# Performance work log

Measured on AMD Instinct MI355X. Metric: run time of the kernel, lower is better.

Reference implementation:

```python
import jax, jax.numpy as jnp
import numpy as np

B, T, D, H = 32, 2048, 1024, 128


def setup_inputs() -> dict:
    key = jax.random.key(0)
    ks = jax.random.split(key, 7)
    s = 1.0 / np.sqrt(D)
    return {
        "x": jax.random.normal(ks[0], (B, T, D), dtype=jnp.float32),
        "Wk": jax.random.normal(ks[1], (D, H), dtype=jnp.float32) * s,
        "bk": jax.random.normal(ks[2], (H,), dtype=jnp.float32) * 0.01,
        "Wq": jax.random.normal(ks[3], (D, H), dtype=jnp.float32) * s,
        "bq": jax.random.normal(ks[4], (H,), dtype=jnp.float32) * 0.01,
        "Wv": jax.random.normal(ks[5], (D, H), dtype=jnp.float32) * s,
        "bv": jax.random.normal(ks[6], (H,), dtype=jnp.float32) * 0.01,
    }


def reference(x, Wk, bk, Wq, bq, Wv, bv):
    # Single causal attention head. NOTE faithful quirk: scores = K @ Q^T.
    k = x @ Wk + bk  # [B,T,H]
    q = x @ Wq + bq  # [B,T,H]
    v = x @ Wv + bv  # [B,T,H]
    scale = k.shape[-1] ** -0.5
    wei = jnp.einsum("bth,bsh->bts", k, q) * scale  # [B,T,T], K on the left
    t = x.shape[1]
    causal = jnp.tril(jnp.ones((t, t), dtype=bool))
    wei = jnp.where(causal, wei, -jnp.inf)
    wei = jax.nn.softmax(wei, axis=-1)
    # dropout is eval-mode identity (deterministic reference)
    out = jnp.einsum("bts,bsh->bth", wei, v)  # [B,T,H]
    return out
```

## Files before the change

kernel.cpp:

```cpp
#include <hip/hip_runtime.h>
#include <hip/hip_bf16.h>
#include <stdint.h>

typedef __bf16 bf16;
typedef __bf16 bf16x8 __attribute__((ext_vector_type(8)));
typedef __bf16 bf16x4 __attribute__((ext_vector_type(4)));
typedef float f32x4 __attribute__((ext_vector_type(4)));
typedef float f32x8 __attribute__((ext_vector_type(8)));

#define BB 32
#define TT 2048
#define DD 1024
#define HH 128
#define SCALE 0.08838834764831845f
#define LOG2E 1.4426950408889634f
#define KS (SCALE * LOG2E)

__device__ __forceinline__ void gl_lds16(const bf16* g, bf16* l) {
  __builtin_amdgcn_global_load_lds((__attribute__((address_space(1))) const void*)g,
                                   (__attribute__((address_space(3))) void*)l,
                                   16, 0, 0);
}

__global__ __launch_bounds__(256) void prep_w(const float* __restrict__ Wk,
                                              const float* __restrict__ Wq,
                                              const float* __restrict__ Wv,
                                              const float* __restrict__ bk,
                                              const float* __restrict__ bq,
                                              const float* __restrict__ bv,
                                              bf16* __restrict__ Wt,
                                              float* __restrict__ bcat) {
  int tid = blockIdx.x * 256 + threadIdx.x;
  if (tid < 384) {
    int mat = tid >> 7, h = tid & 127;
    float bb = (mat == 0) ? bk[h] : (mat == 1) ? bq[h] : bv[h];
    bcat[tid] = (mat == 0) ? bb * KS : bb;
  }
  int mat = tid >> 14;
  int r = tid & 16383;
  int h = r & 127;
  int d0 = (r >> 7) << 3;
  const float* W = (mat == 0) ? Wk : (mat == 1) ? Wq : Wv;
  const float ks = (mat == 0) ? KS : 1.0f;
  bf16x8 v;
#pragma unroll
  for (int i = 0; i < 8; ++i) v[i] = (bf16)(W[(size_t)(d0 + i) * HH + h] * ks);
  *(bf16x8*)(Wt + ((size_t)mat * HH + h) * DD + d0) = v;
}

__global__ __launch_bounds__(512, 2) void qkv_proj(
    const float* __restrict__ x, const bf16* __restrict__ Wt,
    const float* __restrict__ bcat,
    bf16* __restrict__ kb, bf16* __restrict__ qb, bf16* __restrict__ Vt) {
  const int bid = blockIdx.x;
  const int tid = threadIdx.x;
  const int lane = tid & 63;
  const int w = tid >> 6;
  const int wr = w >> 2, wc = w & 3;
  const int l15 = lane & 15, l4 = lane >> 4;
  const size_t row0 = (size_t)bid * 256;
  const int colbase = wc * 96;
  const int rowbase = wr * 128;

  __shared__ __attribute__((aligned(16))) bf16 As[2][256][40];
  __shared__ __attribute__((aligned(16))) bf16 Ws[2][384 * 32];

  const int sxr = tid >> 1, sxh = (tid & 1) * 16;

  f32x4 acc[8][6];
#pragma unroll
  for (int m = 0; m < 8; ++m)
#pragma unroll
    for (int n = 0; n < 6; ++n) acc[m][n] = f32x4{0.f, 0.f, 0.f, 0.f};

  auto stage_w = [&](int buf, int k0) {
#pragma unroll
    for (int i = 0; i < 3; ++i) {
      int base = i * 512 + (w << 6);
      int L = base + lane;
      int col = L >> 2, j = L & 3;
      const bf16* src = Wt + (size_t)col * DD + k0 + ((j ^ ((col >> 1) & 3)) << 3);
      gl_lds16(src, &Ws[buf][0] + (size_t)base * 8);
    }
  };
  auto write_x = [&](int buf, f32x8 a0, f32x8 a1) {
    bf16x8 t0, t1;
#pragma unroll
    for (int i = 0; i < 8; ++i) { t0[i] = (bf16)a0[i]; t1[i] = (bf16)a1[i]; }
    *(bf16x8*)&As[buf][sxr][sxh] = t0;
    *(bf16x8*)&As[buf][sxr][sxh + 8] = t1;
  };

  {
    const float* src = x + (row0 + sxr) * DD + sxh;
    f32x8 a0 = *(const f32x8*)src;
    f32x8 a1 = *(const f32x8*)(src + 8);
    stage_w(0, 0);
    write_x(0, a0, a1);
  }
  __syncthreads();

  for (int step = 0; step < 32; ++step) {
    const int cur = step & 1;
    const int k0 = step * 32;

    f32x8 a0, a1;
    if (step < 31) {
      const float* src = x + (row0 + sxr) * DD + k0 + 32 + sxh;
      a0 = *(const f32x8*)src;
      a1 = *(const f32x8*)(src + 8);
      stage_w(cur ^ 1, k0 + 32);
    }

    bf16x8 bfr[6];
#pragma unroll
    for (int n = 0; n < 6; ++n) {
      int col = colbase + n * 16 + l15;
      bfr[n] = *(const bf16x8*)&Ws[cur][col * 32 + ((l4 ^ ((col >> 1) & 3)) << 3)];
    }
#pragma unroll
    for (int m = 0; m < 8; ++m) {
      int r = rowbase + m * 16 + l15;
      bf16x8 afm = *(const bf16x8*)&As[cur][r][l4 * 8];
#pragma unroll
      for (int n = 0; n < 6; ++n)
        acc[m][n] = __builtin_amdgcn_mfma_f32_16x16x32_bf16(afm, bfr[n],
                                                            acc[m][n], 0, 0, 0);
    }

    if (step < 31) write_x(cur ^ 1, a0, a1);
    __syncthreads();
  }

  float bvv[6];
#pragma unroll
  for (int n = 0; n < 6; ++n) bvv[n] = bcat[colbase + n * 16 + l15];

  const int bidx = bid >> 3;
  const int tloc0 = (bid & 7) * 256;
#pragma unroll
  for (int m = 0; m < 8; ++m)
#pragma unroll
    for (int n = 0; n < 6; ++n) {
      int col = colbase + n * 16 + l15;
      int mat = col >> 7;
      int hcol = col & 127;
      int rloc = rowbase + m * 16 + l4 * 4;
      if (mat == 2) {
        bf16x4 v4;
#pragma unroll
        for (int e = 0; e < 4; ++e) v4[e] = (bf16)(acc[m][n][e] + bvv[n]);
        *(bf16x4*)(Vt + ((size_t)bidx * HH + hcol) * TT + tloc0 + rloc) = v4;
      } else {
        bf16* dst = (mat == 0) ? kb : qb;
#pragma unroll
        for (int e = 0; e < 4; ++e)
          dst[(row0 + rloc + e) * HH + hcol] = (bf16)(acc[m][n][e] + bvv[n]);
      }
    }
}

__global__ __launch_bounds__(256, 3) void attn(const bf16* __restrict__ kb,
                                               const bf16* __restrict__ qb,
                                               const bf16* __restrict__ Vt,
                                               float* __restrict__ out) {
  const int bid = blockIdx.x;
  const int b = bid & 31;
  const int p = bid >> 5;
  const int tid = threadIdx.x;
  const int lane = tid & 63;
  const int w = tid >> 6;
  const int l15 = lane & 15, l4 = lane >> 4;

  __shared__ __attribute__((aligned(16))) bf16 Es[64 * 128];
  __shared__ __attribute__((aligned(16))) bf16 Vs[128 * 64];
  __shared__ __attribute__((aligned(16))) bf16 Ps[4][16 * 72];

  for (int job = 0; job < 2; ++job) {
    const int tile = job ? p : (31 - p);
    const int t0 = tile * 64;

    bf16x8 af[4];
    {
      const bf16* kp = kb + ((size_t)b * TT + t0 + w * 16 + l15) * HH + l4 * 8;
#pragma unroll
      for (int kc = 0; kc < 4; ++kc) af[kc] = *(const bf16x8*)(kp + kc * 32);
    }

    f32x4 o[8];
#pragma unroll
    for (int j = 0; j < 8; ++j) o[j] = f32x4{0.f, 0.f, 0.f, 0.f};
    float mrow[4], lrow[4];
#pragma unroll
    for (int e = 0; e < 4; ++e) { mrow[e] = -1e30f; lrow[e] = 0.f; }

    const int nst = tile + 1;
    for (int jt = 0; jt < nst; ++jt) {
      const int s0 = jt * 64;
      {
        const bf16* Eg = qb + ((size_t)b * TT + s0) * HH;
#pragma unroll
        for (int it = 0; it < 4; ++it) {
          int L = w * 256 + it * 64 + lane;
          int er = L >> 4, ec = L & 15;
          int ecs = ec ^ (er & 7);
          gl_lds16(Eg + er * HH + ecs * 8, Es + (size_t)(w * 256 + it * 64) * 8);
        }
        const bf16* Vg = Vt + (size_t)b * HH * TT + s0;
#pragma unroll
        for (int it = 0; it < 4; ++it) {
          int L = w * 256 + it * 64 + lane;
          int vr = L >> 3, vc = L & 7;
          int vcs = vc ^ (vr & 7);
          gl_lds16(Vg + (size_t)vr * TT + vcs * 8, Vs + (size_t)(w * 256 + it * 64) * 8);
        }
      }
      __syncthreads();

      f32x4 s[4];
#pragma unroll
      for (int j = 0; j < 4; ++j) s[j] = f32x4{0.f, 0.f, 0.f, 0.f};
#pragma unroll
      for (int kc = 0; kc < 4; ++kc) {
        bf16x8 ef[4];
#pragma unroll
        for (int fn = 0; fn < 4; ++fn) {
          int er = fn * 16 + l15;
          int c = kc * 4 + l4;
          int cs = c ^ (er & 7);
          ef[fn] = *(const bf16x8*)&Es[er * 128 + cs * 8];
        }
#pragma unroll
        for (int fn = 0; fn < 4; ++fn)
          s[fn] = __builtin_amdgcn_mfma_f32_16x16x32_bf16(af[kc], ef[fn],
                                                          s[fn], 0, 0, 0);
      }

      if (s0 + 63 > t0 + w * 16) {
#pragma unroll
        for (int fn = 0; fn < 4; ++fn)
#pragma unroll
          for (int e = 0; e < 4; ++e) {
            int tg = t0 + w * 16 + l4 * 4 + e;
            int sg = s0 + fn * 16 + l15;
            if (sg > tg) s[fn][e] = -1e30f;
          }
      }

      float mx[4];
#pragma unroll
      for (int e = 0; e < 4; ++e) {
        float m = fmaxf(fmaxf(s[0][e], s[1][e]), fmaxf(s[2][e], s[3][e]));
#pragma unroll
        for (int d = 1; d < 16; d <<= 1) m = fmaxf(m, __shfl_xor(m, d));
        mx[e] = m;
      }
      float g = fmaxf(fmaxf(mx[0] - mrow[0], mx[1] - mrow[1]),
                      fmaxf(mx[2] - mrow[2], mx[3] - mrow[3]));
      if (!__all(g <= 8.0f)) {
#pragma unroll
        for (int e = 0; e < 4; ++e) {
          float mn = fmaxf(mrow[e], mx[e]);
          float rsc = exp2f(mrow[e] - mn);
          lrow[e] *= rsc;
#pragma unroll
          for (int fh = 0; fh < 8; ++fh) o[fh][e] *= rsc;
          mrow[e] = mn;
        }
      }
#pragma unroll
      for (int e = 0; e < 4; ++e) {
        float ps = 0.f;
#pragma unroll
        for (int fn = 0; fn < 4; ++fn) {
          float pv = exp2f(s[fn][e] - mrow[e]);
          s[fn][e] = pv;
          ps += pv;
        }
#pragma unroll
        for (int d = 1; d < 16; d <<= 1) ps += __shfl_xor(ps, d);
        lrow[e] += ps;
      }

#pragma unroll
      for (int fn = 0; fn < 4; ++fn)
#pragma unroll
        for (int e = 0; e < 4; ++e)
          Ps[w][(l4 * 4 + e) * 72 + fn * 16 + l15] = (bf16)s[fn][e];

#pragma unroll
      for (int kc = 0; kc < 2; ++kc) {
        bf16x8 pf = *(const bf16x8*)&Ps[w][l15 * 72 + kc * 32 + l4 * 8];
#pragma unroll
        for (int fh = 0; fh < 8; ++fh) {
          int vr = fh * 16 + l15;
          int c = kc * 4 + l4;
          int cs = c ^ (vr & 7);
          bf16x8 vf = *(const bf16x8*)&Vs[vr * 64 + cs * 8];
          o[fh] = __builtin_amdgcn_mfma_f32_16x16x32_bf16(pf, vf, o[fh], 0, 0, 0);
        }
      }
      __syncthreads();
    }

#pragma unroll
    for (int e = 0; e < 4; ++e) {
      float rl = 1.0f / lrow[e];
      int tg = t0 + w * 16 + l4 * 4 + e;
#pragma unroll
      for (int fh = 0; fh < 8; ++fh)
        out[((size_t)b * TT + tg) * HH + fh * 16 + l15] = o[fh][e] * rl;
    }
  }
}

extern "C" void kernel_launch(void* const* d_in, const int* in_sizes, int n_in,
                              void* d_out, int out_size, void* d_ws, size_t ws_size,
                              hipStream_t stream) {
  (void)in_sizes; (void)n_in; (void)out_size; (void)ws_size;
  const float* x  = (const float*)d_in[0];
  const float* Wk = (const float*)d_in[1];
  const float* bk = (const float*)d_in[2];
  const float* Wq = (const float*)d_in[3];
  const float* bq = (const float*)d_in[4];
  const float* Wv = (const float*)d_in[5];
  const float* bv = (const float*)d_in[6];
  float* out = (float*)d_out;

  const size_t NTH = (size_t)BB * TT * HH;
  bf16* kb = (bf16*)d_ws;
  bf16* qb = kb + NTH;
  bf16* Vt = qb + NTH;
  bf16* Wt = Vt + NTH;
  float* bcat = (float*)(Wt + (size_t)3 * HH * DD);

  prep_w<<<192, 256, 0, stream>>>(Wk, Wq, Wv, bk, bq, bv, Wt, bcat);
  qkv_proj<<<256, 512, 0, stream>>>(x, Wt, bcat, kb, qb, Vt);
  attn<<<512, 256, 0, stream>>>(kb, qb, Vt, out);
}
```

Baseline: 191.7 us.

## Stage fp32 x tiles into LDS via async global_load_lds with triple buffering

The QKV projection now copies fp32 x tiles straight into LDS with asynchronous global-to-LDS loads, using an XOR-swizzled layout and a three-deep buffer. Conversion to bf16 moves to the point where MFMA operands are read. Synchronisation is rebuilt around explicit vmcnt waits and a single barrier per step, so both x and W loads overlap the matrix math and no longer pass through registers. In exchange, the fp32 triple buffer greatly enlarges shared memory, which may stop two blocks fitting per CU, and the conversion work is repeated by every wave that reads a tile.

Result: slower. 223.9 us (+16.8%).

```diff
diff --git a/kernel.cpp b/kernel.cpp
--- a/kernel.cpp
+++ b/kernel.cpp
@@ -17,6 +17,11 @@
 #define KS (SCALE * LOG2E)
 
 __device__ __forceinline__ void gl_lds16(const bf16* g, bf16* l) {
+  __builtin_amdgcn_global_load_lds((__attribute__((address_space(1))) const void*)g,
+                                   (__attribute__((address_space(3))) void*)l,
+                                   16, 0, 0);
+}
+__device__ __forceinline__ void gl_lds16f(const float* g, float* l) {
   __builtin_amdgcn_global_load_lds((__attribute__((address_space(1))) const void*)g,
                                    (__attribute__((address_space(3))) void*)l,
                                    16, 0, 0);
@@ -62,10 +67,8 @@
   const int colbase = wc * 96;
   const int rowbase = wr * 128;
 
-  __shared__ __attribute__((aligned(16))) bf16 As[2][256][40];
-  __shared__ __attribute__((aligned(16))) bf16 Ws[2][384 * 32];
-
-  const int sxr = tid >> 1, sxh = (tid & 1) * 16;
+  __shared__ __attribute__((aligned(16))) float As[3][256 * 32];
+  __shared__ __attribute__((aligned(16))) bf16  Ws[2][384 * 32];
 
   f32x4 acc[8][6];
 #pragma unroll
@@ -73,64 +76,69 @@
 #pragma unroll
     for (int n = 0; n < 6; ++n) acc[m][n] = f32x4{0.f, 0.f, 0.f, 0.f};
 
-  auto stage_w = [&](int buf, int k0) {
+  auto stage_w = [&](int s) {
+    bf16* dst0 = &Ws[s & 1][0];
 #pragma unroll
     for (int i = 0; i < 3; ++i) {
       int base = i * 512 + (w << 6);
-      int L = base + lane;
-      int col = L >> 2, j = L & 3;
-      const bf16* src = Wt + (size_t)col * DD + k0 + ((j ^ ((col >> 1) & 3)) << 3);
-      gl_lds16(src, &Ws[buf][0] + (size_t)base * 8);
+      int C = base + lane;
+      int col = C >> 2, j = C & 3;
+      const bf16* src = Wt + (size_t)col * DD + s * 32 + ((j ^ ((col >> 1) & 3)) << 3);
+      gl_lds16(src, dst0 + (size_t)base * 8);
     }
   };
-  auto write_x = [&](int buf, f32x8 a0, f32x8 a1) {
-    bf16x8 t0, t1;
-#pragma unroll
-    for (int i = 0; i < 8; ++i) { t0[i] = (bf16)a0[i]; t1[i] = (bf16)a1[i]; }
-    *(bf16x8*)&As[buf][sxr][sxh] = t0;
-    *(bf16x8*)&As[buf][sxr][sxh + 8] = t1;
+  auto stage_x = [&](int s) {
+    float* dst0 = &As[s % 3][0];
+#pragma unroll
+    for (int i = 0; i < 4; ++i) {
+      int base = i * 512 + (w << 6);
+      int C = base + lane;
+      int r = C >> 3, c = C & 7;
+      const float* src = x + (row0 + r) * DD + s * 32 + ((c ^ (r & 7)) << 2);
+      gl_lds16f(src, dst0 + (size_t)base * 4);
+    }
   };
 
-  {
-    const float* src = x + (row0 + sxr) * DD + sxh;
-    f32x8 a0 = *(const f32x8*)src;
-    f32x8 a1 = *(const f32x8*)(src + 8);
-    stage_w(0, 0);
-    write_x(0, a0, a1);
-  }
-  __syncthreads();
-
-  for (int step = 0; step < 32; ++step) {
-    const int cur = step & 1;
-    const int k0 = step * 32;
-
-    f32x8 a0, a1;
-    if (step < 31) {
-      const float* src = x + (row0 + sxr) * DD + k0 + 32 + sxh;
-      a0 = *(const f32x8*)src;
-      a1 = *(const f32x8*)(src + 8);
-      stage_w(cur ^ 1, k0 + 32);
-    }
-
-    bf16x8 bfr[6];
+  auto compute = [&](int t) {
+    const float* Ab = &As[t % 3][0];
+    const bf16* Wb = &Ws[t & 1][0];
+    bf16x8 afm[8];
+#pragma unroll
+    for (int m = 0; m < 8; ++m) {
+      int r = rowbase + m * 16 + l15;
+      int c0 = (l4 * 2) ^ (r & 7), c1 = (l4 * 2 + 1) ^ (r & 7);
+      f32x4 lo = *(const f32x4*)&Ab[r * 32 + c0 * 4];
+      f32x4 hi = *(const f32x4*)&Ab[r * 32 + c1 * 4];
+#pragma unroll
+      for (int i = 0; i < 4; ++i) { afm[m][i] = (bf16)lo[i]; afm[m][4 + i] = (bf16)hi[i]; }
+    }
 #pragma unroll
     for (int n = 0; n < 6; ++n) {
       int col = colbase + n * 16 + l15;
-      bfr[n] = *(const bf16x8*)&Ws[cur][col * 32 + ((l4 ^ ((col >> 1) & 3)) << 3)];
-    }
-#pragma unroll
-    for (int m = 0; m < 8; ++m) {
-      int r = rowbase + m * 16 + l15;
-      bf16x8 afm = *(const bf16x8*)&As[cur][r][l4 * 8];
-#pragma unroll
-      for (int n = 0; n < 6; ++n)
-        acc[m][n] = __builtin_amdgcn_mfma_f32_16x16x32_bf16(afm, bfr[n],
+      bf16x8 bfr = *(const bf16x8*)&Wb[col * 32 + ((l4 ^ ((col >> 1) & 3)) << 3)];
+#pragma unroll
+      for (int m = 0; m < 8; ++m)
+        acc[m][n] = __builtin_amdgcn_mfma_f32_16x16x32_bf16(afm[m], bfr,
                                                             acc[m][n], 0, 0, 0);
     }
-
-    if (step < 31) write_x(cur ^ 1, a0, a1);
-    __syncthreads();
+  };
+
+  stage_w(0);
+  stage_x(0);
+  stage_x(1);
+
+  for (int t = 0; t < 31; ++t) {
+    asm volatile("s_waitcnt vmcnt(4)" ::: "memory");
+    __builtin_amdgcn_s_barrier();
+    __builtin_amdgcn_sched_barrier(0);
+    stage_w(t + 1);
+    if (t + 2 < 32) stage_x(t + 2);
+    compute(t);
   }
+  asm volatile("s_waitcnt vmcnt(0)" ::: "memory");
+  __builtin_amdgcn_s_barrier();
+  __builtin_amdgcn_sched_barrier(0);
+  compute(31);
 
   float bvv[6];
 #pragma unroll
```

## Shrink QKV projection tile to 64 rows and stage x in half-K chunks

Applied to the files above, without the earlier changes.

The QKV projection now uses 64-row tiles instead of 256, launching 1024 blocks rather than 256 so more CUs have work. It loads a full 512-wide half of x per row into swizzled LDS in one go, replacing the per-step x double buffering. Only the weight tiles stay double-buffered, and plain __syncthreads is replaced by explicit vmcnt waits plus barriers. The weight matrix is reread from L2 four times as often, and each wave does less MFMA work per LDS load.

Result: slower. 258.8 us (+35.0%).

```diff
diff --git a/kernel.cpp b/kernel.cpp
--- a/kernel.cpp
+++ b/kernel.cpp
@@ -21,6 +21,12 @@
                                    (__attribute__((address_space(3))) void*)l,
                                    16, 0, 0);
 }
+
+#define KBAR(N) do { \
+  asm volatile("s_waitcnt vmcnt(" #N ") lgkmcnt(0)" ::: "memory"); \
+  __builtin_amdgcn_s_barrier(); \
+  __builtin_amdgcn_sched_barrier(0); \
+} while (0)
 
 __global__ __launch_bounds__(256) void prep_w(const float* __restrict__ Wk,
                                               const float* __restrict__ Wq,
@@ -58,88 +64,93 @@
   const int w = tid >> 6;
   const int wr = w >> 2, wc = w & 3;
   const int l15 = lane & 15, l4 = lane >> 4;
-  const size_t row0 = (size_t)bid * 256;
+  const size_t row0 = (size_t)bid * 64;
   const int colbase = wc * 96;
-  const int rowbase = wr * 128;
-
-  __shared__ __attribute__((aligned(16))) bf16 As[2][256][40];
+  const int rowbase = wr * 32;
+
+  __shared__ __attribute__((aligned(16))) bf16 As[64 * 512];
   __shared__ __attribute__((aligned(16))) bf16 Ws[2][384 * 32];
 
-  const int sxr = tid >> 1, sxh = (tid & 1) * 16;
-
-  f32x4 acc[8][6];
-#pragma unroll
-  for (int m = 0; m < 8; ++m)
+  const int sxr = tid >> 3;
+  const int sxs = tid & 7;
+
+  f32x4 acc[2][6];
+#pragma unroll
+  for (int m = 0; m < 2; ++m)
 #pragma unroll
     for (int n = 0; n < 6; ++n) acc[m][n] = f32x4{0.f, 0.f, 0.f, 0.f};
 
-  auto stage_w = [&](int buf, int k0) {
+  auto stage_w = [&](int s, int buf) {
+    bf16* dst0 = &Ws[buf][0];
 #pragma unroll
     for (int i = 0; i < 3; ++i) {
       int base = i * 512 + (w << 6);
-      int L = base + lane;
-      int col = L >> 2, j = L & 3;
-      const bf16* src = Wt + (size_t)col * DD + k0 + ((j ^ ((col >> 1) & 3)) << 3);
-      gl_lds16(src, &Ws[buf][0] + (size_t)base * 8);
+      int C = base + lane;
+      int col = C >> 2, j = C & 3;
+      const bf16* src = Wt + (size_t)col * DD + s * 32 + ((j ^ ((col >> 1) & 3)) << 3);
+      gl_lds16(src, dst0 + (size_t)base * 8);
     }
   };
-  auto write_x = [&](int buf, f32x8 a0, f32x8 a1) {
-    bf16x8 t0, t1;
-#pragma unroll
-    for (int i = 0; i < 8; ++i) { t0[i] = (bf16)a0[i]; t1[i] = (bf16)a1[i]; }
-    *(bf16x8*)&As[buf][sxr][sxh] = t0;
-    *(bf16x8*)&As[buf][sxr][sxh + 8] = t1;
+  auto load_x = [&](int half, f32x8* xv) {
+    const float* xp = x + (row0 + sxr) * DD + half * 512 + sxs * 64;
+#pragma unroll
+    for (int i = 0; i < 8; ++i) xv[i] = *(const f32x8*)(xp + i * 8);
   };
-
-  {
-    const float* src = x + (row0 + sxr) * DD + sxh;
-    f32x8 a0 = *(const f32x8*)src;
-    f32x8 a1 = *(const f32x8*)(src + 8);
-    stage_w(0, 0);
-    write_x(0, a0, a1);
-  }
-  __syncthreads();
-
-  for (int step = 0; step < 32; ++step) {
-    const int cur = step & 1;
-    const int k0 = step * 32;
-
-    f32x8 a0, a1;
-    if (step < 31) {
-      const float* src = x + (row0 + sxr) * DD + k0 + 32 + sxh;
-      a0 = *(const f32x8*)src;
-      a1 = *(const f32x8*)(src + 8);
-      stage_w(cur ^ 1, k0 + 32);
-    }
-
-    bf16x8 bfr[6];
+  auto cvt_write = [&](const f32x8* xv) {
+#pragma unroll
+    for (int i = 0; i < 8; ++i) {
+      bf16x8 t;
+#pragma unroll
+      for (int j = 0; j < 8; ++j) t[j] = (bf16)xv[i][j];
+      int c = sxs * 8 + i;
+      *(bf16x8*)&As[sxr * 512 + ((c ^ (sxr & 7)) << 3)] = t;
+    }
+  };
+  auto kstep = [&](int half, int s) {
+    if (s < 15) stage_w(half * 16 + s + 1, (s + 1) & 1);
+    bf16x8 afm[2], bfr[6];
+#pragma unroll
+    for (int m = 0; m < 2; ++m) {
+      int r = rowbase + m * 16 + l15;
+      int c = s * 4 + l4;
+      afm[m] = *(const bf16x8*)&As[r * 512 + ((c ^ (r & 7)) << 3)];
+    }
 #pragma unroll
     for (int n = 0; n < 6; ++n) {
       int col = colbase + n * 16 + l15;
-      bfr[n] = *(const bf16x8*)&Ws[cur][col * 32 + ((l4 ^ ((col >> 1) & 3)) << 3)];
-    }
-#pragma unroll
-    for (int m = 0; m < 8; ++m) {
-      int r = rowbase + m * 16 + l15;
-      bf16x8 afm = *(const bf16x8*)&As[cur][r][l4 * 8];
+      bfr[n] = *(const bf16x8*)&Ws[s & 1][col * 32 + ((l4 ^ ((col >> 1) & 3)) << 3)];
+    }
+#pragma unroll
+    for (int m = 0; m < 2; ++m)
 #pragma unroll
       for (int n = 0; n < 6; ++n)
-        acc[m][n] = __builtin_amdgcn_mfma_f32_16x16x32_bf16(afm, bfr[n],
+        acc[m][n] = __builtin_amdgcn_mfma_f32_16x16x32_bf16(afm[m], bfr[n],
                                                             acc[m][n], 0, 0, 0);
-    }
-
-    if (step < 31) write_x(cur ^ 1, a0, a1);
-    __syncthreads();
-  }
+  };
+
+  f32x8 xv[8];
+  load_x(0, xv);
+  stage_w(0, 0);
+  cvt_write(xv);
+  load_x(1, xv);
+  KBAR(8);
+
+  for (int s = 0; s < 16; ++s) { kstep(0, s); KBAR(8); }
+
+  stage_w(16, 0);
+  cvt_write(xv);
+  KBAR(0);
+
+  for (int s = 0; s < 16; ++s) { kstep(1, s); KBAR(0); }
 
   float bvv[6];
 #pragma unroll
   for (int n = 0; n < 6; ++n) bvv[n] = bcat[colbase + n * 16 + l15];
 
-  const int bidx = bid >> 3;
-  const int tloc0 = (bid & 7) * 256;
-#pragma unroll
-  for (int m = 0; m < 8; ++m)
+  const int bidx = bid >> 5;
+  const int tloc0 = (bid & 31) * 64;
+#pragma unroll
+  for (int m = 0; m < 2; ++m)
 #pragma unroll
     for (int n = 0; n < 6; ++n) {
       int col = colbase + n * 16 + l15;
@@ -335,6 +346,6 @@
   float* bcat = (float*)(Wt + (size_t)3 * HH * DD);
 
   prep_w<<<192, 256, 0, stream>>>(Wk, Wq, Wv, bk, bq, bv, Wt, bcat);
-  qkv_proj<<<256, 512, 0, stream>>>(x, Wt, bcat, kb, qb, Vt);
+  qkv_proj<<<1024, 512, 0, stream>>>(x, Wt, bcat, kb, qb, Vt);
   attn<<<512, 256, 0, stream>>>(kb, qb, Vt, out);
 }
```

## Split QKV projection into smaller row/column tiles with swizzled x LDS layout

Applied to the files above, without the earlier changes.

Retiles the QKV projection GEMM from 256 blocks of 256 rows by 384 columns into 1024 blocks of 128 rows by 192 columns with 256 threads each. The aim is more blocks per CU, better occupancy and load balance. The padded x tile in LDS is also replaced with an XOR-swizzled layout to avoid bank conflicts. In exchange, each x tile is read from global memory twice, once per column half, which raises memory traffic on a memory-heavy step.

Result: slower. 253.0 us (+32.0%).

```diff
diff --git a/kernel.cpp b/kernel.cpp
--- a/kernel.cpp
+++ b/kernel.cpp
@@ -48,53 +48,64 @@
   *(bf16x8*)(Wt + ((size_t)mat * HH + h) * DD + d0) = v;
 }
 
-__global__ __launch_bounds__(512, 2) void qkv_proj(
+__global__ __launch_bounds__(256, 3) void qkv_proj(
     const float* __restrict__ x, const bf16* __restrict__ Wt,
     const float* __restrict__ bcat,
     bf16* __restrict__ kb, bf16* __restrict__ qb, bf16* __restrict__ Vt) {
   const int bid = blockIdx.x;
+  const int mtile = bid >> 1;
+  const int nh = bid & 1;
   const int tid = threadIdx.x;
   const int lane = tid & 63;
   const int w = tid >> 6;
-  const int wr = w >> 2, wc = w & 3;
+  const int wr = w >> 1, wc = w & 1;
   const int l15 = lane & 15, l4 = lane >> 4;
-  const size_t row0 = (size_t)bid * 256;
+  const size_t row0 = (size_t)mtile * 128;
+  const int ncol0 = nh * 192;
   const int colbase = wc * 96;
-  const int rowbase = wr * 128;
-
-  __shared__ __attribute__((aligned(16))) bf16 As[2][256][40];
-  __shared__ __attribute__((aligned(16))) bf16 Ws[2][384 * 32];
-
-  const int sxr = tid >> 1, sxh = (tid & 1) * 16;
-
-  f32x4 acc[8][6];
-#pragma unroll
-  for (int m = 0; m < 8; ++m)
+  const int rowbase = wr * 64;
+
+  __shared__ __attribute__((aligned(16))) bf16 As[2][128 * 32];
+  __shared__ __attribute__((aligned(16))) bf16 Ws[2][192 * 32];
+
+  const int sxr = tid >> 1;
+  const int sxh = tid & 1;
+
+  f32x4 acc[4][6];
+#pragma unroll
+  for (int m = 0; m < 4; ++m)
 #pragma unroll
     for (int n = 0; n < 6; ++n) acc[m][n] = f32x4{0.f, 0.f, 0.f, 0.f};
 
   auto stage_w = [&](int buf, int k0) {
+    bf16* dst0 = &Ws[buf][0];
 #pragma unroll
     for (int i = 0; i < 3; ++i) {
-      int base = i * 512 + (w << 6);
-      int L = base + lane;
-      int col = L >> 2, j = L & 3;
-      const bf16* src = Wt + (size_t)col * DD + k0 + ((j ^ ((col >> 1) & 3)) << 3);
-      gl_lds16(src, &Ws[buf][0] + (size_t)base * 8);
-    }
+      int base = i * 256 + (w << 6);
+      int C = base + lane;
+      int col = C >> 2, j = C & 3;
+      const bf16* src = Wt + (size_t)(ncol0 + col) * DD + k0 +
+                        ((j ^ ((col >> 1) & 3)) << 3);
+      gl_lds16(src, dst0 + (size_t)base * 8);
+    }
+  };
+  auto load_x = [&](int k0, f32x8& a0, f32x8& a1) {
+    const float* src = x + (row0 + sxr) * DD + k0 + sxh * 16;
+    a0 = *(const f32x8*)src;
+    a1 = *(const f32x8*)(src + 8);
   };
   auto write_x = [&](int buf, f32x8 a0, f32x8 a1) {
     bf16x8 t0, t1;
 #pragma unroll
     for (int i = 0; i < 8; ++i) { t0[i] = (bf16)a0[i]; t1[i] = (bf16)a1[i]; }
-    *(bf16x8*)&As[buf][sxr][sxh] = t0;
-    *(bf16x8*)&As[buf][sxr][sxh + 8] = t1;
+    int c0 = (sxh * 2) ^ (sxr & 3), c1 = (sxh * 2 + 1) ^ (sxr & 3);
+    *(bf16x8*)&As[buf][sxr * 32 + (c0 << 3)] = t0;
+    *(bf16x8*)&As[buf][sxr * 32 + (c1 << 3)] = t1;
   };
 
   {
-    const float* src = x + (row0 + sxr) * DD + sxh;
-    f32x8 a0 = *(const f32x8*)src;
-    f32x8 a1 = *(const f32x8*)(src + 8);
+    f32x8 a0, a1;
+    load_x(0, a0, a1);
     stage_w(0, 0);
     write_x(0, a0, a1);
   }
@@ -102,31 +113,30 @@
 
   for (int step = 0; step < 32; ++step) {
     const int cur = step & 1;
-    const int k0 = step * 32;
 
     f32x8 a0, a1;
     if (step < 31) {
-      const float* src = x + (row0 + sxr) * DD + k0 + 32 + sxh;
-      a0 = *(const f32x8*)src;
-      a1 = *(const f32x8*)(src + 8);
-      stage_w(cur ^ 1, k0 + 32);
-    }
-
-    bf16x8 bfr[6];
+      load_x((step + 1) * 32, a0, a1);
+      stage_w(cur ^ 1, (step + 1) * 32);
+    }
+
+    bf16x8 afm[4], bfr[6];
+#pragma unroll
+    for (int m = 0; m < 4; ++m) {
+      int r = rowbase + m * 16 + l15;
+      afm[m] = *(const bf16x8*)&As[cur][r * 32 + ((l4 ^ (r & 3)) << 3)];
+    }
 #pragma unroll
     for (int n = 0; n < 6; ++n) {
-      int col = colbase + n * 16 + l15;
-      bfr[n] = *(const bf16x8*)&Ws[cur][col * 32 + ((l4 ^ ((col >> 1) & 3)) << 3)];
-    }
-#pragma unroll
-    for (int m = 0; m < 8; ++m) {
-      int r = rowbase + m * 16 + l15;
-      bf16x8 afm = *(const bf16x8*)&As[cur][r][l4 * 8];
+      int cl = colbase + n * 16 + l15;
+      bfr[n] = *(const bf16x8*)&Ws[cur][cl * 32 + ((l4 ^ ((cl >> 1) & 3)) << 3)];
+    }
+#pragma unroll
+    for (int m = 0; m < 4; ++m)
 #pragma unroll
       for (int n = 0; n < 6; ++n)
-        acc[m][n] = __builtin_amdgcn_mfma_f32_16x16x32_bf16(afm, bfr[n],
+        acc[m][n] = __builtin_amdgcn_mfma_f32_16x16x32_bf16(afm[m], bfr[n],
                                                             acc[m][n], 0, 0, 0);
-    }
 
     if (step < 31) write_x(cur ^ 1, a0, a1);
     __syncthreads();
@@ -134,15 +144,15 @@
 
   float bvv[6];
 #pragma unroll
-  for (int n = 0; n < 6; ++n) bvv[n] = bcat[colbase + n * 16 + l15];
-
-  const int bidx = bid >> 3;
-  const int tloc0 = (bid & 7) * 256;
-#pragma unroll
-  for (int m = 0; m < 8; ++m)
+  for (int n = 0; n < 6; ++n) bvv[n] = bcat[ncol0 + colbase + n * 16 + l15];
+
+  const int bidx = mtile >> 4;
+  const int tloc0 = (mtile & 15) * 128;
+#pragma unroll
+  for (int m = 0; m < 4; ++m)
 #pragma unroll
     for (int n = 0; n < 6; ++n) {
-      int col = colbase + n * 16 + l15;
+      int col = ncol0 + colbase + n * 16 + l15;
       int mat = col >> 7;
       int hcol = col & 127;
       int rloc = rowbase + m * 16 + l4 * 4;
@@ -335,6 +345,6 @@
   float* bcat = (float*)(Wt + (size_t)3 * HH * DD);
 
   prep_w<<<192, 256, 0, stream>>>(Wk, Wq, Wv, bk, bq, bv, Wt, bcat);
-  qkv_proj<<<256, 512, 0, stream>>>(x, Wt, bcat, kb, qb, Vt);
+  qkv_proj<<<1024, 256, 0, stream>>>(x, Wt, bcat, kb, qb, Vt);
   attn<<<512, 256, 0, stream>>>(kb, qb, Vt, out);
 }
```
